# Kernel tuning notes

Measured on AMD Instinct MI355X. Metric: run time of the kernel, lower is better.

Reference implementation:

```python
import jax, jax.numpy as jnp
import numpy as np

B, N, C, T, K = 32, 512, 64, 24, 3
F_OUT = 64
EPS = 1e-5


def setup_inputs() -> dict:
    key = jax.random.key(0)
    ks = jax.random.split(key, 20)
    u = lambda k, shape: jax.random.uniform(k, shape, jnp.float32, -0.1, 0.1)
    xav = lambda k, shape, fi, fo: jax.random.uniform(k, shape, jnp.float32, -1.0, 1.0) * np.sqrt(6.0 / (fi + fo))
    inp = {
        "x": jax.random.normal(ks[0], (B, N, C, T), jnp.float32),
        "cheb_polys": jax.random.normal(ks[1], (K, N, N), jnp.float32) / np.sqrt(N),
        # SpatialAttention params (in_features)
        "W1": u(ks[2], (T,)),
        "W2": u(ks[3], (C, T)),
        "W3": u(ks[4], (C,)),
        "bs": u(ks[5], (N, N)),
        "Vs": u(ks[6], (N, N)),
        # TemporalAttention params (out_features)
        "U1": u(ks[7], (N,)),
        "U2": u(ks[8], (F_OUT, N)),
        "U3": u(ks[9], (F_OUT,)),
        "be": u(ks[10], (1, T, T)),
        "Ve": u(ks[11], (T, T)),
        # ChebConv
        "Theta": xav(ks[12], (K, C, F_OUT), C, F_OUT),
        # temporal Conv2d (kernel (1,3), pad (0,1))
        "conv_w": xav(ks[13], (F_OUT, F_OUT, 1, 3), F_OUT * 3, F_OUT * 3),
        "conv_b": jnp.zeros((F_OUT,), jnp.float32),
        # LayerNorm
        "ln_w": jnp.ones((F_OUT,), jnp.float32),
        "ln_b": jnp.zeros((F_OUT,), jnp.float32),
    }
    return inp


def reference(x, cheb_polys, W1, W2, W3, bs, Vs, U1, U2, U3, be, Ve, Theta, conv_w, conv_b, ln_w, ln_b):
    # ---- Spatial attention: x (B,N,C,T) -> S (B,N,N)
    lhs = jnp.einsum('bnct,t->bnc', x, W1) @ W2          # (B,N,T)
    rhs = jnp.einsum('bnct,c->bnt', x, W3)               # (B,N,T)
    product = jnp.einsum('bmt,bnt->bmn', lhs, rhs)       # (B,N,N)
    S = jnp.einsum('mn,bnk->bmk', Vs, jax.nn.sigmoid(product + bs))
    S = jax.nn.softmax(S, axis=-1)

    # ---- Spatial mixing + Chebyshev graph conv + ReLU (vectorized over T)
    x_s = jnp.einsum('bmn,bnct->bmct', S, x)             # (B,N,C,T)
    g = jnp.einsum('kmn,bnct->kbmct', cheb_polys, x_s)   # (K,B,N,C,T)
    h = jax.nn.relu(jnp.einsum('kbmct,kcf->bmft', g, Theta))  # (B,N,F,T)

    # ---- Temporal attention: h -> E (B,T,T)
    lhs_t = jnp.einsum('bnft,n->btf', h, U1) @ U2        # (B,T,N)
    rhs_t = jnp.einsum('f,bnft->bnt', U3, h)             # (B,N,T)
    prod_t = jnp.einsum('btn,bns->bts', lhs_t, rhs_t)    # (B,T,T)
    E = jnp.einsum('ts,bsr->btr', Ve, jax.nn.sigmoid(prod_t + be))
    E = jax.nn.softmax(E, axis=-1)

    # ---- Temporal mixing
    h = jnp.einsum('bnft,bts->bnfs', h, E)               # (B,N,F,T)

    # ---- Temporal conv2d: (B,F,N,T), kernel (1,3), padding (0,1)
    h_perm = jnp.transpose(h, (0, 2, 1, 3))
    h_perm = jax.lax.conv_general_dilated(
        h_perm, conv_w, window_strides=(1, 1), padding=((0, 0), (1, 1)),
        dimension_numbers=('NCHW', 'OIHW', 'NCHW'))
    h_perm = h_perm + conv_b[None, :, None, None]
    h = jnp.transpose(h_perm, (0, 2, 1, 3))              # (B,N,F,T)

    # ---- Residual (Identity since in_features == out_features) + LayerNorm over F
    combined = jnp.transpose(h + x, (0, 1, 3, 2))        # (B,N,T,F)
    mu = jnp.mean(combined, axis=-1, keepdims=True)
    var = jnp.var(combined, axis=-1, keepdims=True)
    normed = (combined - mu) * jax.lax.rsqrt(var + EPS) * ln_w + ln_b
    return jnp.transpose(normed, (0, 1, 3, 2))           # (B,N,F,T)
```

## Files before the change

### kernel.cpp

```cpp
#include <hip/hip_runtime.h>

constexpr int cB = 32, cN = 512, cC = 64, cT = 24, cK = 3, cF = 64;
constexpr int cCT = cC * cT;
constexpr int cFT = cF * cT;

typedef __attribute__((ext_vector_type(8))) short s16x8;
typedef __attribute__((ext_vector_type(8))) unsigned short u16x8;
typedef __attribute__((ext_vector_type(4))) float f32x4;

__device__ inline unsigned short f2bf(float f) {
    union { float f; unsigned int u; } v; v.f = f;
    unsigned int r = v.u + 0x7FFFu + ((v.u >> 16) & 1u);
    return (unsigned short)(r >> 16);
}
__device__ inline float bf2f(unsigned short u) {
    union { unsigned int i; float f; } v; v.i = ((unsigned int)u) << 16;
    return v.f;
}

__global__ __launch_bounds__(64) void k_spatial_lr(
    const float* __restrict__ x, const float* __restrict__ W1,
    const float* __restrict__ W2, const float* __restrict__ W3,
    float* __restrict__ lhs, float* __restrict__ rhs)
{
    int bn = blockIdx.x;
    int tid = threadIdx.x;
    __shared__ float xs[64][25];
    __shared__ float a_sh[64];
    const float* xp = x + (size_t)bn * cCT;
    for (int i = tid; i < cCT; i += 64) xs[i / cT][i % cT] = xp[i];
    __syncthreads();
    float s = 0.f;
    #pragma unroll
    for (int t = 0; t < cT; t++) s += xs[tid][t] * W1[t];
    a_sh[tid] = s;
    __syncthreads();
    if (tid < cT) {
        float l = 0.f, r = 0.f;
        for (int c = 0; c < cC; c++) {
            l += a_sh[c] * W2[c * cT + tid];
            r += xs[c][tid] * W3[c];
        }
        lhs[(size_t)bn * cT + tid] = l;
        rhs[(size_t)bn * cT + tid] = r;
    }
}

__global__ __launch_bounds__(256) void k_product_t(
    const float* __restrict__ lhs, const float* __restrict__ rhs,
    const float* __restrict__ bs, unsigned short* __restrict__ Pt)
{
    int b = blockIdx.z;
    int m0 = blockIdx.y * 16, n0 = blockIdx.x * 16;
    int tx = threadIdx.x, ty = threadIdx.y;
    int tid = ty * 16 + tx;
    __shared__ float L[16][25], R[16][25], bss[16][17];
    for (int i = tid; i < 16 * cT; i += 256) {
        int r = i / cT, c = i % cT;
        L[r][c] = lhs[((size_t)b * cN + m0 + r) * cT + c];
        R[r][c] = rhs[((size_t)b * cN + n0 + r) * cT + c];
    }
    bss[tid >> 4][tid & 15] = bs[(size_t)(m0 + (tid >> 4)) * cN + n0 + (tid & 15)];
    __syncthreads();
    float s = 0.f;
    #pragma unroll
    for (int t = 0; t < cT; t++) s += L[tx][t] * R[ty][t];
    s += bss[tx][ty];
    float sig = 1.f / (1.f + expf(-s));
    Pt[((size_t)b * cN + n0 + ty) * cN + m0 + tx] = f2bf(sig);
}

template<int CM>
__global__ __launch_bounds__(256) void k_mfma_gemm(
    const unsigned short* __restrict__ A, int lda, long long aB, long long segA,
    const unsigned short* __restrict__ Bt, int ldb, long long bB, long long segB,
    void* __restrict__ Cv, int ldc, long long cBs,
    int K, int doAcc, int doRelu, int nx, int ny)
{
    __shared__ unsigned short As[128][40];
    __shared__ unsigned short Bs[128][40];
    int tid = threadIdx.x;
    int nb = gridDim.x;
    int bid = blockIdx.x;
    int xcd = bid & 7, loc = bid >> 3;
    int nid = xcd * (nb >> 3) + loc;
    int z   = nid / (nx * ny);
    int rem = nid % (nx * ny);
    int bm  = (rem / nx) * 128;
    int bn  = (rem % nx) * 128;

    const unsigned short* Ap = A  + (size_t)z * aB;
    const unsigned short* Bp = Bt + (size_t)z * bB;

    int lane = tid & 63, w = tid >> 6;
    int wm = (w >> 1) * 64, wn = (w & 1) * 64;
    int fr = lane & 15, kg = (lane >> 4) * 8;

    f32x4 acc[4][4] = {};

    int c0 = tid, c1 = tid + 256;
    int r0 = c0 >> 2, g0 = (c0 & 3) * 8;
    int r1 = c1 >> 2, g1 = (c1 & 3) * 8;

    for (int k0 = 0; k0 < K; k0 += 32) {
        int seg = k0 >> 9, off = k0 & 511;
        const unsigned short* Aseg = Ap + (size_t)seg * segA;
        const unsigned short* Bseg = Bp + (size_t)seg * segB;
        u16x8 a0 = *(const u16x8*)(Aseg + (size_t)(bm + r0) * lda + off + g0);
        u16x8 a1 = *(const u16x8*)(Aseg + (size_t)(bm + r1) * lda + off + g1);
        u16x8 b0 = *(const u16x8*)(Bseg + (size_t)(bn + r0) * ldb + off + g0);
        u16x8 b1 = *(const u16x8*)(Bseg + (size_t)(bn + r1) * ldb + off + g1);
        __syncthreads();
        *(u16x8*)&As[r0][g0] = a0;
        *(u16x8*)&As[r1][g1] = a1;
        *(u16x8*)&Bs[r0][g0] = b0;
        *(u16x8*)&Bs[r1][g1] = b1;
        __syncthreads();
        s16x8 af[4], bf[4];
        #pragma unroll
        for (int i = 0; i < 4; i++)
            af[i] = *(const s16x8*)&As[wm + i * 16 + fr][kg];
        #pragma unroll
        for (int j = 0; j < 4; j++)
            bf[j] = *(const s16x8*)&Bs[wn + j * 16 + fr][kg];
        #pragma unroll
        for (int i = 0; i < 4; i++)
            #pragma unroll
            for (int j = 0; j < 4; j++)
                acc[i][j] = __builtin_amdgcn_mfma_f32_16x16x32_bf16(
                    af[i], bf[j], acc[i][j], 0, 0, 0);
    }
    int rb = (lane >> 4) * 4;
    if (CM == 0) {
        float* Cp = (float*)Cv + (size_t)z * cBs;
        #pragma unroll
        for (int i = 0; i < 4; i++) {
            int row = bm + wm + i * 16 + rb;
            #pragma unroll
            for (int j = 0; j < 4; j++) {
                int col = bn + wn + j * 16 + fr;
                #pragma unroll
                for (int r = 0; r < 4; r++) {
                    size_t idx = (size_t)(row + r) * ldc + col;
                    float v = acc[i][j][r];
                    if (doAcc) v += Cp[idx];
                    if (doRelu) v = fmaxf(v, 0.f);
                    Cp[idx] = v;
                }
            }
        }
    } else {
        unsigned short* Cp = (unsigned short*)Cv + (size_t)z * cBs;
        #pragma unroll
        for (int i = 0; i < 4; i++) {
            int row = bm + wm + i * 16 + rb;
            #pragma unroll
            for (int j = 0; j < 4; j++) {
                int col = bn + wn + j * 16 + fr;
                #pragma unroll
                for (int r = 0; r < 4; r++) {
                    float v = acc[i][j][r];
                    if (doRelu) v = fmaxf(v, 0.f);
                    Cp[(size_t)(row + r) * ldc + col] = f2bf(v);
                }
            }
        }
    }
}

__global__ __launch_bounds__(256) void k_softmax512(float* __restrict__ S)
{
    int row = blockIdx.x;
    int tid = threadIdx.x;
    float* p = S + (size_t)row * cN;
    float v0 = p[tid], v1 = p[tid + 256];
    __shared__ float red[256];
    red[tid] = fmaxf(v0, v1);
    __syncthreads();
    for (int off = 128; off > 0; off >>= 1) {
        if (tid < off) red[tid] = fmaxf(red[tid], red[tid + off]);
        __syncthreads();
    }
    float mx = red[0];
    __syncthreads();
    float e0 = expf(v0 - mx), e1 = expf(v1 - mx);
    red[tid] = e0 + e1;
    __syncthreads();
    for (int off = 128; off > 0; off >>= 1) {
        if (tid < off) red[tid] += red[tid + off];
        __syncthreads();
    }
    float inv = 1.f / red[0];
    p[tid] = e0 * inv;
    p[tid + 256] = e1 * inv;
}

__global__ __launch_bounds__(256) void k_transpose_S(
    const float* __restrict__ S0, unsigned short* __restrict__ St)
{
    int b = blockIdx.z;
    int q0 = blockIdx.y * 64, n0 = blockIdx.x * 64;
    __shared__ float t[64][68];
    int tid = threadIdx.x;
    int r = tid >> 2, grp = (tid & 3) * 16;
    const float* ip = S0 + ((size_t)b * cN + q0 + r) * cN + n0 + grp;
    #pragma unroll
    for (int i = 0; i < 16; i += 4)
        *(float4*)&t[r][grp + i] = *(const float4*)(ip + i);
    __syncthreads();
    int nr = tid & 63, qg = (tid >> 6) * 16;
    unsigned short* op = St + ((size_t)b * cN + n0 + nr) * cN + q0 + qg;
    u16x8 v0, v1;
    #pragma unroll
    for (int i = 0; i < 8; i++) {
        v0[i] = f2bf(t[qg + i][nr]);
        v1[i] = f2bf(t[qg + 8 + i][nr]);
    }
    *(u16x8*)op = v0;
    *(u16x8*)(op + 8) = v1;
}

__global__ __launch_bounds__(64) void k_xtrans_half(
    const float* __restrict__ x, int half, unsigned short* __restrict__ xT2)
{
    int idx = blockIdx.x;
    int z = idx >> 9, n = idx & 511;
    int b = half * 16 + z;
    int tid = threadIdx.x;
    __shared__ float xs[64][25];
    const float* xp = x + (size_t)(b * (size_t)cN + n) * cCT;
    for (int i = tid; i < cCT; i += 64) xs[i / cT][i % cT] = xp[i];
    __syncthreads();
    unsigned short* op = xT2 + (size_t)z * 786432 + (size_t)n * 64;
    for (int i = tid; i < cCT; i += 64) {
        int t = i >> 6, c = i & 63;
        op[(size_t)t * 32768 + c] = f2bf(xs[c][t]);
    }
}

__global__ __launch_bounds__(256) void k_xtheta_mfma(
    const unsigned short* __restrict__ xT2,
    const unsigned short* __restrict__ ThT,
    unsigned short* __restrict__ XTt,
    long long segX)
{
    __shared__ unsigned short As[128][72];
    __shared__ unsigned short Ths[64][72];
    __shared__ unsigned short Cs[64][136];
    int tid = threadIdx.x;
    int n0 = blockIdx.x * 128;
    int t  = blockIdx.y;
    int z  = blockIdx.z;

    const unsigned short* ap = xT2 + (size_t)z * 786432 + (size_t)t * 32768 + n0 * 64;
    #pragma unroll
    for (int it = 0; it < 4; it++) {
        int v = tid + it * 256;
        int row = v >> 3, c8 = (v & 7) * 8;
        *(u16x8*)&As[row][c8] = *(const u16x8*)(ap + row * 64 + c8);
    }

    int lane = tid & 63, w = tid >> 6;
    int fr = lane & 15, kg = (lane >> 4) * 8;
    int rb = (lane >> 4) * 4;

    for (int k = 0; k < cK; k++) {
        __syncthreads();
        #pragma unroll
        for (int it = 0; it < 2; it++) {
            int vi = tid + it * 256;
            int row = vi >> 3, c8 = (vi & 7) * 8;
            *(u16x8*)&Ths[row][c8] =
                *(const u16x8*)(ThT + (size_t)k * 4096 + row * 64 + c8);
        }
        __syncthreads();
        f32x4 acc[2][4] = {};
        #pragma unroll
        for (int ks = 0; ks < 2; ks++) {
            s16x8 af[2], bf[4];
            #pragma unroll
            for (int i = 0; i < 2; i++)
                af[i] = *(const s16x8*)&As[w * 32 + i * 16 + fr][ks * 32 + kg];
            #pragma unroll
            for (int j = 0; j < 4; j++)
                bf[j] = *(const s16x8*)&Ths[j * 16 + fr][ks * 32 + kg];
            #pragma unroll
            for (int i = 0; i < 2; i++)
                #pragma unroll
                for (int j = 0; j < 4; j++)
                    acc[i][j] = __builtin_amdgcn_mfma_f32_16x16x32_bf16(
                        af[i], bf[j], acc[i][j], 0, 0, 0);
        }
        #pragma unroll
        for (int i = 0; i < 2; i++) {
            int rowb = w * 32 + i * 16 + rb;
            #pragma unroll
            for (int j = 0; j < 4; j++) {
                int f = j * 16 + fr;
                #pragma unroll
                for (int r = 0; r < 4; r++)
                    Cs[f][rowb + r] = f2bf(acc[i][j][r]);
            }
        }
        __syncthreads();
        unsigned short* op = XTt + (size_t)k * segX + (size_t)z * 786432 + n0;
        #pragma unroll
        for (int it = 0; it < 4; it++) {
            int v = tid + it * 256;
            int f = v >> 4, n8 = (v & 15) * 8;
            *(u16x8*)(op + (size_t)(f * 24 + t) * 512 + n8) = *(const u16x8*)&Cs[f][n8];
        }
    }
}

__global__ void k_convert(const float* __restrict__ a,
                          unsigned short* __restrict__ o, int n)
{
    int i = blockIdx.x * 256 + threadIdx.x;
    if (i < n) o[i] = f2bf(a[i]);
}

__global__ void k_wprep(const float* __restrict__ cw,
                        unsigned short* __restrict__ W2g)
{
    int i = blockIdx.x * 256 + threadIdx.x;
    if (i < 64 * 192) {
        int f = i / 192, k = i % 192;
        int d = k >> 6, fi = k & 63;
        W2g[i] = f2bf(cw[f * 192 + fi * 3 + d]);
    }
}

__global__ void k_thprep(const float* __restrict__ Theta,
                         unsigned short* __restrict__ ThT)
{
    int i = blockIdx.x * 256 + threadIdx.x;
    if (i < cK * 64 * 64) {
        int k = i >> 12, r = i & 4095;
        int f = r >> 6, c = r & 63;
        ThT[i] = f2bf(Theta[k * 4096 + c * 64 + f]);
    }
}

__global__ __launch_bounds__(256) void k_hU1_part(
    const unsigned short* __restrict__ h, const float* __restrict__ U1,
    float* __restrict__ part)
{
    int b = blockIdx.x, nc = blockIdx.y;
    int tid = threadIdx.x;
    int f = tid & 63, q = tid >> 6;
    float acc[24];
    #pragma unroll
    for (int t = 0; t < 24; t++) acc[t] = 0.f;
    for (int n = nc * 32 + q; n < nc * 32 + 32; n += 4) {
        float u = U1[n];
        const u16x8* hp = (const u16x8*)(h + (((size_t)b * cN + n) * cF + f) * cT);
        #pragma unroll
        for (int v8 = 0; v8 < 3; v8++) {
            u16x8 hv = hp[v8];
            #pragma unroll
            for (int e = 0; e < 8; e++)
                acc[v8 * 8 + e] += u * bf2f(hv[e]);
        }
    }
    __shared__ float ps[4][64][25];
    #pragma unroll
    for (int t = 0; t < 24; t++) ps[q][f][t] = acc[t];
    __syncthreads();
    for (int i = tid; i < cFT; i += 256) {
        int f2 = i / cT, t2 = i % cT;
        float s = ps[0][f2][t2] + ps[1][f2][t2] + ps[2][f2][t2] + ps[3][f2][t2];
        part[(((size_t)b * 16 + nc) * cF + f2) * cT + t2] = s;
    }
}

__global__ __launch_bounds__(256) void k_lhs_t(
    const float* __restrict__ part, const float* __restrict__ U2,
    float* __restrict__ lhs_t)
{
    int b = blockIdx.x, ch = blockIdx.y;
    int tid = threadIdx.x;
    __shared__ float hu[1536];
    for (int i = tid; i < 1536; i += 256) {
        float s = 0.f;
        for (int nc = 0; nc < 16; nc++)
            s += part[((size_t)b * 16 + nc) * 1536 + i];
        hu[i] = s;
    }
    __syncthreads();
    int nn0 = ch * 128;
    for (int i = tid; i < cT * 128; i += 256) {
        int t = i / 128, nn = nn0 + (i % 128);
        float s = 0.f;
        #pragma unroll
        for (int f = 0; f < 64; f++) s += hu[f * cT + t] * U2[(size_t)f * cN + nn];
        lhs_t[((size_t)b * cT + t) * cN + nn] = s;
    }
}

__global__ __launch_bounds__(64) void k_rhs_t(
    const unsigned short* __restrict__ h, const float* __restrict__ U3,
    float* __restrict__ rhs_t)
{
    int bn = blockIdx.x;
    int f = threadIdx.x;
    __shared__ float sl[64][25];
    const u16x8* hp = (const u16x8*)(h + (size_t)bn * cFT + f * cT);
    float u = U3[f];
    #pragma unroll
    for (int v8 = 0; v8 < 3; v8++) {
        u16x8 hv = hp[v8];
        #pragma unroll
        for (int e = 0; e < 8; e++)
            sl[f][v8 * 8 + e] = u * bf2f(hv[e]);
    }
    __syncthreads();
    if (f < cT) {
        float s = 0.f;
        #pragma unroll
        for (int c = 0; c < 64; c++) s += sl[c][f];
        rhs_t[(size_t)bn * cT + f] = s;
    }
}

__global__ __launch_bounds__(576) void k_E(
    const float* __restrict__ lhs_t, const float* __restrict__ rhs_t,
    const float* __restrict__ be, const float* __restrict__ Ve,
    float* __restrict__ E)
{
    int b = blockIdx.x;
    int tid = threadIdx.x;
    int i = tid / 24, j = tid % 24;
    __shared__ float ps[24][25];
    __shared__ float er[24][25];
    __shared__ float mrow[24], srow[24];
    const float* lp = lhs_t + ((size_t)b * cT + i) * cN;
    const float* rp = rhs_t + (size_t)b * cN * cT;
    float s = 0.f;
    for (int n = 0; n < cN; n++) s += lp[n] * rp[n * cT + j];
    s += be[i * cT + j];
    ps[i][j] = 1.f / (1.f + expf(-s));
    __syncthreads();
    float e = 0.f;
    #pragma unroll
    for (int ss = 0; ss < cT; ss++) e += Ve[i * cT + ss] * ps[ss][j];
    er[i][j] = e;
    __syncthreads();
    if (j == 0) {
        float m = -1e30f;
        for (int r = 0; r < cT; r++) m = fmaxf(m, er[i][r]);
        float sm = 0.f;
        for (int r = 0; r < cT; r++) sm += expf(er[i][r] - m);
        mrow[i] = m;
        srow[i] = sm;
    }
    __syncthreads();
    E[(size_t)b * cT * cT + i * cT + j] = expf(er[i][j] - mrow[i]) / srow[i];
}

__global__ __launch_bounds__(256) void k_tmix_mfma(
    const unsigned short* __restrict__ h,
    const float* __restrict__ E,
    unsigned short* __restrict__ hT)
{
    __shared__ float Es[24][25];
    __shared__ unsigned short bounce[8][24][64];
    int tid = threadIdx.x;
    int blk = blockIdx.x;
    int b = blk >> 6;
    int n0 = (blk & 63) * 8;
    for (int i = tid; i < 576; i += 256)
        Es[i / 24][i % 24] = E[(size_t)b * 576 + i];
    __syncthreads();

    int lane = tid & 63, w = tid >> 6;
    int fr = lane & 15, g = lane >> 4;

    s16x8 afr[2];
    #pragma unroll
    for (int m = 0; m < 2; m++) {
        int so = m * 16 + fr;
        u16x8 a = {};
        if (so < 24 && g < 3) {
            #pragma unroll
            for (int e = 0; e < 8; e++)
                a[e] = f2bf(Es[g * 8 + e][so]);
        }
        afr[m] = *(s16x8*)&a;
    }

    f32x4 zero = {};
    #pragma unroll
    for (int ss = 0; ss < 2; ss++) {
        int s = w * 2 + ss;
        const unsigned short* hp = h + ((size_t)b * cN + n0 + s) * cFT;
        #pragma unroll
        for (int jj = 0; jj < 4; jj++) {
            u16x8 bfrag = {};
            if (g < 3)
                bfrag = *(const u16x8*)(hp + (jj * 16 + fr) * 24 + g * 8);
            s16x8 bf = *(s16x8*)&bfrag;
            #pragma unroll
            for (int m = 0; m < 2; m++) {
                f32x4 c = __builtin_amdgcn_mfma_f32_16x16x32_bf16(
                    afr[m], bf, zero, 0, 0, 0);
                #pragma unroll
                for (int r = 0; r < 4; r++) {
                    int so = m * 16 + g * 4 + r;
                    if (so < 24)
                        bounce[s][so][jj * 16 + fr] = f2bf(c[r]);
                }
            }
        }
    }
    __syncthreads();
    unsigned short* op = hT + ((size_t)b * cN + n0) * cFT;
    #pragma unroll
    for (int it = 0; it < 6; it++) {
        int i = tid + it * 256;
        *(u16x8*)(op + i * 8) = *(const u16x8*)&bounce[0][0][i * 8];
    }
}

__global__ __launch_bounds__(256) void k_convmfma(
    const unsigned short* __restrict__ hT,
    const float* __restrict__ x,
    const unsigned short* __restrict__ W2g,
    const float* __restrict__ cb,
    const float* __restrict__ lnw, const float* __restrict__ lnb,
    float* __restrict__ out)
{
    __shared__ unsigned short Hs[8][26][72];
    __shared__ unsigned short Ws[64][200];
    int tid = threadIdx.x;
    int blk = blockIdx.x;
    int b = blk >> 6;
    int n0 = (blk & 63) * 8;
    const unsigned short* hp = hT + ((size_t)b * cN + n0) * cFT;

    #pragma unroll
    for (int it = 0; it < 6; it++) {
        int v = tid + it * 256;
        int s = v / 192;
        int r = v % 192;
        int t = r >> 3, f0 = (r & 7) * 8;
        u16x8 val = *(const u16x8*)(hp + (size_t)s * cFT + t * 64 + f0);
        *(u16x8*)&Hs[s][1 + t][f0] = val;
    }
    if (tid < 144) {
        int s = tid / 18, rm = tid % 18;
        int side = rm / 9, c8 = (rm % 9) * 8;
        u16x8 z = {};
        *(u16x8*)&Hs[s][side * 25][c8] = z;
    }
    #pragma unroll
    for (int it = 0; it < 48; it++) {
        int i = tid + it * 256;
        Ws[i / 192][i % 192] = W2g[i];
    }
    __syncthreads();

    int lane = tid & 63, w = tid >> 6;
    int fr = lane & 15, kgrp = lane >> 4;
    f32x4 acc[3][4] = {};

    int sA[3], tA[3];
    #pragma unroll
    for (int mi = 0; mi < 3; mi++) {
        int row = (w * 3 + mi) * 16 + fr;
        sA[mi] = row / 24; tA[mi] = row % 24;
    }
    #pragma unroll
    for (int ks = 0; ks < 6; ks++) {
        int d = ks >> 1;
        int fi0 = (ks & 1) * 32 + kgrp * 8;
        s16x8 bf[4];
        #pragma unroll
        for (int j = 0; j < 4; j++)
            bf[j] = *(const s16x8*)&Ws[j * 16 + fr][ks * 32 + kgrp * 8];
        #pragma unroll
        for (int mi = 0; mi < 3; mi++) {
            s16x8 af = *(const s16x8*)&Hs[sA[mi]][tA[mi] + d][fi0];
            #pragma unroll
            for (int j = 0; j < 4; j++)
                acc[mi][j] = __builtin_amdgcn_mfma_f32_16x16x32_bf16(
                    af, bf[j], acc[mi][j], 0, 0, 0);
        }
    }

    float lnw_v[4], lnb_v[4], cb_v[4];
    #pragma unroll
    for (int j = 0; j < 4; j++) {
        int f = j * 16 + fr;
        lnw_v[j] = lnw[f]; lnb_v[j] = lnb[f]; cb_v[j] = cb[f];
    }
    #pragma unroll
    for (int mi = 0; mi < 3; mi++) {
        int rowbase = (w * 3 + mi) * 16 + kgrp * 4;
        int sB = rowbase / 24, tb = rowbase % 24;
        size_t slab = ((size_t)b * cN + n0 + sB) * 64;
        float outv[4][4];
        #pragma unroll
        for (int r = 0; r < 4; r++) {
            int t = tb + r;
            float v[4], s1 = 0.f, s2 = 0.f;
            #pragma unroll
            for (int j = 0; j < 4; j++) {
                float xres = x[(slab + j * 16 + fr) * 24 + t];
                v[j] = acc[mi][j][r] + cb_v[j] + xres;
                s1 += v[j];
                s2 += v[j] * v[j];
            }
            #pragma unroll
            for (int off = 1; off < 16; off <<= 1) {
                s1 += __shfl_xor(s1, off, 64);
                s2 += __shfl_xor(s2, off, 64);
            }
            float mean = s1 * (1.f / 64.f);
            float var = s2 * (1.f / 64.f) - mean * mean;
            float rstd = rsqrtf(var + 1e-5f);
            #pragma unroll
            for (int j = 0; j < 4; j++)
                outv[j][r] = (v[j] - mean) * rstd * lnw_v[j] + lnb_v[j];
        }
        #pragma unroll
        for (int j = 0; j < 4; j++) {
            float4 o = make_float4(outv[j][0], outv[j][1], outv[j][2], outv[j][3]);
            *(float4*)&out[(slab + j * 16 + fr) * 24 + tb] = o;
        }
    }
}

extern "C" void kernel_launch(void* const* d_in, const int* in_sizes, int n_in,
                              void* d_out, int out_size, void* d_ws, size_t ws_size,
                              hipStream_t stream)
{
    const float* x     = (const float*)d_in[0];
    const float* cheb  = (const float*)d_in[1];
    const float* W1    = (const float*)d_in[2];
    const float* W2    = (const float*)d_in[3];
    const float* W3    = (const float*)d_in[4];
    const float* bs    = (const float*)d_in[5];
    const float* Vs    = (const float*)d_in[6];
    const float* U1    = (const float*)d_in[7];
    const float* U2    = (const float*)d_in[8];
    const float* U3    = (const float*)d_in[9];
    const float* be    = (const float*)d_in[10];
    const float* Ve    = (const float*)d_in[11];
    const float* Theta = (const float*)d_in[12];
    const float* cw    = (const float*)d_in[13];
    const float* cbp   = (const float*)d_in[14];
    const float* lnw   = (const float*)d_in[15];
    const float* lnb   = (const float*)d_in[16];
    float* out = (float*)d_out;
    float* ws  = (float*)d_ws;

    unsigned short* Vs_bf   = (unsigned short*)(ws);
    unsigned short* cheb_bf = (unsigned short*)(ws + 131072);
    float*  lhs  = ws + 524288;
    float*  rhs  = ws + 917504;
    float*  part = ws + 1310720;
    unsigned short* ThT = (unsigned short*)(ws + 1310720);
    float*  Ebuf = ws + 2097152;
    unsigned short* W2g = (unsigned short*)(ws + 2115584);
    unsigned short* St  = (unsigned short*)(ws + 2124800);
    unsigned short* Wk  = (unsigned short*)(ws + 6319104);
    unsigned short* XTt = (unsigned short*)(ws + 12610560);
    unsigned short* Pt  = (unsigned short*)(ws + 12610560);
    float*          S0  = ws + 22047744;
    unsigned short* xT2 = (unsigned short*)(ws + 31484928);
    unsigned short* hbf = (unsigned short*)out;
    unsigned short* hT  = XTt;

    const long long NN2 = (long long)cN * cN;
    const long long NFT = (long long)cN * cFT;
    const long long segW = 16LL * NN2;
    const long long segX = 16LL * 1536 * 512;

    k_convert<<<1024, 256, 0, stream>>>(Vs, Vs_bf, 262144);
    k_convert<<<3072, 256, 0, stream>>>(cheb, cheb_bf, 786432);
    k_wprep<<<48, 256, 0, stream>>>(cw, W2g);
    k_thprep<<<48, 256, 0, stream>>>(Theta, ThT);

    k_spatial_lr<<<cB * cN, 64, 0, stream>>>(x, W1, W2, W3, lhs, rhs);
    k_product_t<<<dim3(32, 32, cB), dim3(16, 16), 0, stream>>>(lhs, rhs, bs, Pt);
    k_mfma_gemm<0><<<512, 256, 0, stream>>>(
        Vs_bf, 512, 0LL, 0LL, Pt, 512, NN2, 0LL, S0, 512, NN2, 512, 0, 0, 4, 4);
    k_softmax512<<<cB * cN, 256, 0, stream>>>(S0);
    k_transpose_S<<<dim3(8, 8, cB), 256, 0, stream>>>(S0, St);

    for (int half = 0; half < 2; half++) {
        k_xtrans_half<<<16 * 512, 64, 0, stream>>>(x, half, xT2);
        k_xtheta_mfma<<<dim3(4, 24, 16), 256, 0, stream>>>(xT2, ThT, XTt, segX);
        for (int k = 0; k < cK; k++) {
            k_mfma_gemm<1><<<256, 256, 0, stream>>>(
                cheb_bf + (size_t)k * NN2, 512, 0LL, 0LL,
                St + (size_t)half * 16 * NN2, 512, NN2, 0LL,
                Wk + (size_t)k * segW, 512, NN2, 512, 0, 0, 4, 4);
        }
        k_mfma_gemm<1><<<768, 256, 0, stream>>>(
            Wk, 512, NN2, segW, XTt, 512, 786432LL, segX,
            hbf + (size_t)half * 16 * NFT, 1536, NFT, 1536, 0, 1, 12, 4);
    }

    k_hU1_part<<<dim3(cB, 16), 256, 0, stream>>>(hbf, U1, part);
    k_rhs_t<<<cB * cN, 64, 0, stream>>>(hbf, U3, rhs);
    k_lhs_t<<<dim3(cB, 4), 256, 0, stream>>>(part, U2, lhs);
    k_E<<<cB, 576, 0, stream>>>(lhs, rhs, be, Ve, Ebuf);

    k_tmix_mfma<<<2048, 256, 0, stream>>>(hbf, Ebuf, hT);
    k_convmfma<<<2048, 256, 0, stream>>>(hT, x, W2g, cbp, lnw, lnb, out);
}
```

Measured before the change: 532.9 us.

## Batch cheb-poly GEMMs into one launch, vectorize x loads, cache rhs_t in LDS

Merges the three per-order Chebyshev GEMM launches into one launch that covers all K orders by treating the concatenated cheb matrices as a taller A operand. This changes the Wk layout to an interleaved [b][3*512][512] form and updates the follow-on GEMM strides to match. Separately, k_spatial_lr now handles four (b,n) rows per 256-thread block using float4 loads, k_xtrans_half uses float4 loads, and k_E stages rhs_t in shared memory. The main aim is fewer launches and better memory coalescing. The risk is that the layout and stride changes must line up exactly with what the GEMM template expects.

Result: faster. 476.9 us (-10.5%).

```diff
diff --git a/kernel.cpp b/kernel.cpp
--- a/kernel.cpp
+++ b/kernel.cpp
@@ -18,31 +18,39 @@
     return v.f;
 }
 
-__global__ __launch_bounds__(64) void k_spatial_lr(
+__global__ __launch_bounds__(256) void k_spatial_lr(
     const float* __restrict__ x, const float* __restrict__ W1,
     const float* __restrict__ W2, const float* __restrict__ W3,
     float* __restrict__ lhs, float* __restrict__ rhs)
 {
-    int bn = blockIdx.x;
-    int tid = threadIdx.x;
-    __shared__ float xs[64][25];
-    __shared__ float a_sh[64];
-    const float* xp = x + (size_t)bn * cCT;
-    for (int i = tid; i < cCT; i += 64) xs[i / cT][i % cT] = xp[i];
-    __syncthreads();
+    int tid = threadIdx.x;
+    int bn0 = blockIdx.x * 4;
+    __shared__ float xs[4][64][25];
+    __shared__ float a_sh[4][64];
+    const float4* xp4 = (const float4*)(x + (size_t)bn0 * cCT);
+    for (int v = tid; v < 1536; v += 256) {
+        int sl = v / 384, i = v % 384;
+        float4 f4 = xp4[sl * 384 + i];
+        int e = i * 4;
+        int c = e / 24, t0 = e % 24;
+        xs[sl][c][t0] = f4.x; xs[sl][c][t0 + 1] = f4.y;
+        xs[sl][c][t0 + 2] = f4.z; xs[sl][c][t0 + 3] = f4.w;
+    }
+    __syncthreads();
+    int sl = tid >> 6, c = tid & 63;
     float s = 0.f;
     #pragma unroll
-    for (int t = 0; t < cT; t++) s += xs[tid][t] * W1[t];
-    a_sh[tid] = s;
-    __syncthreads();
-    if (tid < cT) {
+    for (int t = 0; t < cT; t++) s += xs[sl][c][t] * W1[t];
+    a_sh[sl][c] = s;
+    __syncthreads();
+    if (c < cT) {
         float l = 0.f, r = 0.f;
-        for (int c = 0; c < cC; c++) {
-            l += a_sh[c] * W2[c * cT + tid];
-            r += xs[c][tid] * W3[c];
-        }
-        lhs[(size_t)bn * cT + tid] = l;
-        rhs[(size_t)bn * cT + tid] = r;
+        for (int cp = 0; cp < cC; cp++) {
+            l += a_sh[sl][cp] * W2[cp * cT + c];
+            r += xs[sl][cp][c] * W3[cp];
+        }
+        lhs[(size_t)(bn0 + sl) * cT + c] = l;
+        rhs[(size_t)(bn0 + sl) * cT + c] = r;
     }
 }
 
@@ -228,8 +236,14 @@
     int b = half * 16 + z;
     int tid = threadIdx.x;
     __shared__ float xs[64][25];
-    const float* xp = x + (size_t)(b * (size_t)cN + n) * cCT;
-    for (int i = tid; i < cCT; i += 64) xs[i / cT][i % cT] = xp[i];
+    const float4* xp4 = (const float4*)(x + (size_t)(b * (size_t)cN + n) * cCT);
+    for (int i = tid; i < 384; i += 64) {
+        float4 f4 = xp4[i];
+        int e = i * 4;
+        int c = e / 24, t0 = e % 24;
+        xs[c][t0] = f4.x; xs[c][t0 + 1] = f4.y;
+        xs[c][t0 + 2] = f4.z; xs[c][t0 + 3] = f4.w;
+    }
     __syncthreads();
     unsigned short* op = xT2 + (size_t)z * 786432 + (size_t)n * 64;
     for (int i = tid; i < cCT; i += 64) {
@@ -431,13 +445,16 @@
     int b = blockIdx.x;
     int tid = threadIdx.x;
     int i = tid / 24, j = tid % 24;
+    __shared__ float rs[12288];
     __shared__ float ps[24][25];
     __shared__ float er[24][25];
     __shared__ float mrow[24], srow[24];
+    const float* rp = rhs_t + (size_t)b * 12288;
+    for (int v = tid; v < 12288; v += 576) rs[v] = rp[v];
+    __syncthreads();
     const float* lp = lhs_t + ((size_t)b * cT + i) * cN;
-    const float* rp = rhs_t + (size_t)b * cN * cT;
     float s = 0.f;
-    for (int n = 0; n < cN; n++) s += lp[n] * rp[n * cT + j];
+    for (int n = 0; n < cN; n++) s += lp[n] * rs[n * cT + j];
     s += be[i * cT + j];
     ps[i][j] = 1.f / (1.f + expf(-s));
     __syncthreads();
@@ -674,7 +691,6 @@
 
     const long long NN2 = (long long)cN * cN;
     const long long NFT = (long long)cN * cFT;
-    const long long segW = 16LL * NN2;
     const long long segX = 16LL * 1536 * 512;
 
     k_convert<<<1024, 256, 0, stream>>>(Vs, Vs_bf, 262144);
@@ -682,7 +698,7 @@
     k_wprep<<<48, 256, 0, stream>>>(cw, W2g);
     k_thprep<<<48, 256, 0, stream>>>(Theta, ThT);
 
-    k_spatial_lr<<<cB * cN, 64, 0, stream>>>(x, W1, W2, W3, lhs, rhs);
+    k_spatial_lr<<<cB * cN / 4, 256, 0, stream>>>(x, W1, W2, W3, lhs, rhs);
     k_product_t<<<dim3(32, 32, cB), dim3(16, 16), 0, stream>>>(lhs, rhs, bs, Pt);
     k_mfma_gemm<0><<<512, 256, 0, stream>>>(
         Vs_bf, 512, 0LL, 0LL, Pt, 512, NN2, 0LL, S0, 512, NN2, 512, 0, 0, 4, 4);
@@ -692,14 +708,12 @@
     for (int half = 0; half < 2; half++) {
         k_xtrans_half<<<16 * 512, 64, 0, stream>>>(x, half, xT2);
         k_xtheta_mfma<<<dim3(4, 24, 16), 256, 0, stream>>>(xT2, ThT, XTt, segX);
-        for (int k = 0; k < cK; k++) {
-            k_mfma_gemm<1><<<256, 256, 0, stream>>>(
-                cheb_bf + (size_t)k * NN2, 512, 0LL, 0LL,
-                St + (size_t)half * 16 * NN2, 512, NN2, 0LL,
-                Wk + (size_t)k * segW, 512, NN2, 512, 0, 0, 4, 4);
-        }
         k_mfma_gemm<1><<<768, 256, 0, stream>>>(
-            Wk, 512, NN2, segW, XTt, 512, 786432LL, segX,
+            cheb_bf, 512, 0LL, 0LL,
+            St + (size_t)half * 16 * NN2, 512, NN2, 0LL,
+            Wk, 512, 3 * NN2, 512, 0, 0, 4, 12);
+        k_mfma_gemm<1><<<768, 256, 0, stream>>>(
+            Wk, 512, 3 * NN2, NN2, XTt, 512, 786432LL, segX,
             hbf + (size_t)half * 16 * NFT, 1536, NFT, 1536, 0, 1, 12, 4);
     }
 
```
